# Performance work log

Hardware: AMD Instinct MI355X
Metric: run time of the kernel (lower is better)

## Reference

```python
import jax, jax.numpy as jnp
import numpy as np

B, N, K, E, H, V = 128, 256, 4, 300, 150, 32000  # batch, nodes/tree, max children, embed, hidden, vocab
DELTA = 1.0


def setup_inputs() -> dict:
    key = jax.random.key(0)
    ks = jax.random.split(key, 8)
    query = jax.random.randint(ks[0], (B, N), 0, V, dtype=jnp.int32)
    pos = jax.random.randint(ks[1], (B, N), 0, V, dtype=jnp.int32)
    neg = jax.random.randint(ks[2], (B, N), 0, V, dtype=jnp.int32)
    # Complete K-ary tree over N nodes: children of node t are {K*t+1, ..., K*t+K} < N; root = node 0.
    ch = np.full((N, K), -1, dtype=np.int32)
    for t in range(N):
        for j in range(K):
            c = K * t + 1 + j
            if c < N:
                ch[t, j] = c
    children = jnp.asarray(ch)
    emb = jax.random.normal(ks[3], (V, E), dtype=jnp.float32) * 0.02
    W_iou = jax.random.normal(ks[4], (E, 3 * H), dtype=jnp.float32) * 0.05
    U_iou = jax.random.normal(ks[5], (H, 3 * H), dtype=jnp.float32) * 0.05
    b_iou = jnp.zeros((3 * H,), jnp.float32)
    W_f = jax.random.normal(ks[6], (E, H), dtype=jnp.float32) * 0.05
    U_f = jax.random.normal(ks[7], (H, H), dtype=jnp.float32) * 0.05
    b_f = jnp.zeros((H,), jnp.float32)
    return {"query": query, "pos": pos, "neg": neg, "children": children,
            "emb": emb, "W_iou": W_iou, "U_iou": U_iou, "b_iou": b_iou,
            "W_f": W_f, "U_f": U_f, "b_f": b_f}


def _childsum_treelstm(x, children, W_iou, U_iou, b_iou, W_f, U_f, b_f):
    """x: [B, N, E] node embeddings. Returns root (c, h): each [B, H]."""
    Bn, Nn, _ = x.shape
    Hh = U_f.shape[0]
    h0 = jnp.zeros((Bn, Nn, Hh), x.dtype)
    c0 = jnp.zeros((Bn, Nn, Hh), x.dtype)

    def step(carry, t):
        h_all, c_all = carry
        ch = children[t]                        # [K] child indices, -1 = padding
        mask = (ch >= 0)
        idx = jnp.where(mask, ch, 0)
        m = mask.astype(x.dtype)[None, :, None]  # [1, K, 1]
        h_k = h_all[:, idx] * m                 # [B, K, H]
        c_k = c_all[:, idx] * m
        h_sum = h_k.sum(axis=1)                 # child-sum h_tilde [B, H]
        x_t = x[:, t]                           # [B, E]
        iou = x_t @ W_iou + h_sum @ U_iou + b_iou
        i, o, u = jnp.split(iou, 3, axis=-1)
        i = jax.nn.sigmoid(i)
        o = jax.nn.sigmoid(o)
        u = jnp.tanh(u)
        # per-child forget gates: f_jk = sigmoid(W_f x_j + U_f h_k + b_f)
        f = jax.nn.sigmoid((x_t @ W_f + b_f)[:, None, :] + h_k @ U_f)  # [B, K, H]
        c_t = i * u + (f * c_k).sum(axis=1)     # c_k already masked
        h_t = o * jnp.tanh(c_t)
        return (h_all.at[:, t].set(h_t), c_all.at[:, t].set(c_t)), None

    # children have larger indices than parents -> process N-1 .. 0 (root last)
    (h_all, c_all), _ = jax.lax.scan(step, (h0, c0), jnp.arange(Nn - 1, -1, -1))
    return c_all[:, 0], h_all[:, 0]


def _cosine(a, b):
    num = (a * b).sum(-1)
    den = jnp.sqrt((a * a).sum(-1) * (b * b).sum(-1)) + 1e-8
    return num / den


def reference(query, pos, neg, children, emb, W_iou, U_iou, b_iou, W_f, U_f, b_f):
    qc, _ = _childsum_treelstm(emb[query], children, W_iou, U_iou, b_iou, W_f, U_f, b_f)
    pc, _ = _childsum_treelstm(emb[pos], children, W_iou, U_iou, b_iou, W_f, U_f, b_f)
    nc, _ = _childsum_treelstm(emb[neg], children, W_iou, U_iou, b_iou, W_f, U_f, b_f)
    a = _cosine(qc, pc)  # [B]
    b = _cosine(qc, nc)  # [B]
    return jax.nn.relu(DELTA - a + b)
```

## Files before the change

kernel.cpp:

```cpp
#include <hip/hip_runtime.h>
#include <hip/hip_bf16.h>

typedef short short8 __attribute__((ext_vector_type(8)));
typedef float floatx4 __attribute__((ext_vector_type(4)));
typedef unsigned short ushort;

#define Bb 128
#define Nn 256
#define Hh 150
#define HK 160
#define Vv 32000
#define NROW 384
#define PROJC 600
#define NINT 64
#define ZROW (Vv + NROW * NINT)

#define WTN 640

__device__ __forceinline__ float sigf(float x) { return 1.0f / (1.0f + __expf(-x)); }
__device__ __forceinline__ float tanhf_(float x) { return 1.0f - 2.0f / (__expf(2.0f * x) + 1.0f); }
__device__ __forceinline__ float bf2f(ushort s) { union { float f; unsigned u; } v; v.u = ((unsigned)s) << 16; return v.f; }
__device__ __forceinline__ ushort f2bf(float f) { __hip_bfloat16 h = __float2bfloat16(f); return *(ushort*)&h; }

__global__ __launch_bounds__(256) void k_prep(
    const float* __restrict__ W_iou, const float* __restrict__ W_f,
    const float* __restrict__ U_iou, const float* __restrict__ U_f,
    const float* __restrict__ b_iou, const float* __restrict__ b_f,
    short* __restrict__ Wt, short* __restrict__ Uti, short* __restrict__ Utf,
    float* __restrict__ biasw, ushort* __restrict__ h_u, float* __restrict__ c_u)
{
    int idx = blockIdx.x * 256 + threadIdx.x;
    const int nWt = 320 * WTN, nUi = 160 * 464, nUf = 160 * 160;
    if (idx < nWt) {
        int k = idx / WTN, n = idx % WTN;
        float v = 0.f;
        if (k < 300) { if (n < 450) v = W_iou[k * 450 + n]; else if (n < 600) v = W_f[k * 150 + (n - 450)]; }
        Wt[n * 320 + k] = (short)f2bf(v);
    } else if (idx < nWt + nUi) {
        int i2 = idx - nWt; int k = i2 / 464, n = i2 % 464;
        float v = (k < 150 && n < 450) ? U_iou[k * 450 + n] : 0.f;
        Uti[n * 160 + k] = (short)f2bf(v);
    } else if (idx < nWt + nUi + nUf) {
        int i2 = idx - nWt - nUi; int k = i2 / 160, n = i2 % 160;
        float v = (k < 150 && n < 150) ? U_f[k * 150 + n] : 0.f;
        Utf[n * 160 + k] = (short)f2bf(v);
    } else if (idx < nWt + nUi + nUf + WTN) {
        int n = idx - nWt - nUi - nUf;
        biasw[n] = n < 450 ? b_iou[n] : (n < 600 ? b_f[n - 450] : 0.f);
    } else if (idx < nWt + nUi + nUf + WTN + HK) {
        int k = idx - (nWt + nUi + nUf + WTN);
        h_u[(long)ZROW * HK + k] = 0;
        c_u[(long)ZROW * HK + k] = 0.f;
    }
}

__global__ __launch_bounds__(256) void k_vproj(
    const float* __restrict__ emb, const short* __restrict__ Wt,
    const float* __restrict__ biasw, ushort* __restrict__ proj)
{
    __shared__ __align__(16) short As[2][32][328];
    const int tid = threadIdx.x;

    const int bid = blockIdx.x;
    const int xcd = bid & 7, li = bid >> 3;
    const int wgid = (xcd < 4 ? xcd * 63 : 252 + (xcd - 4) * 62) + li;

    const int cg = wgid % 5;
    const int rg = wgid / 5;
    const int rowbase = rg * 320;

    const int w = tid >> 6, lane = tid & 63;
    const int m = lane & 15, kq = (lane >> 4) * 8;
    const int t0 = cg * 8 + w * 2;
    const int col0 = t0 * 16 + m;
    const int col1 = col0 + 16;

    short8 bq0[10], bq1[10];
    #pragma unroll
    for (int ks = 0; ks < 10; ks++) {
        bq0[ks] = *(const short8*)(Wt + (long)col0 * 320 + kq + ks * 32);
        bq1[ks] = *(const short8*)(Wt + (long)col1 * 320 + kq + ks * 32);
    }
    const float bias0 = biasw[col0];
    const float bias1 = biasw[col1];

    for (int i = tid; i < 2 * 32 * 5; i += 256) {
        int bz = i / 160, r2 = (i % 160) / 5, kk = (i % 5) * 4;
        *(short4*)&As[bz][r2][300 + kk] = make_short4(0, 0, 0, 0);
    }

    {
        const float4* src = (const float4*)emb + (long)rowbase * 75;
        for (int i = tid; i < 2400; i += 256) {
            int r = i / 75, k0 = (i % 75) * 4;
            float4 x = src[i];
            short4 sv;
            sv.x = (short)f2bf(x.x); sv.y = (short)f2bf(x.y);
            sv.z = (short)f2bf(x.z); sv.w = (short)f2bf(x.w);
            *(short4*)&As[0][r][k0] = sv;
        }
    }
    __syncthreads();

    for (int c = 0; c < 10; c++) {
        const int buf = c & 1;

        float4 x[10];
        if (c < 9) {
            const float4* src = (const float4*)emb + (long)(rowbase + (c + 1) * 32) * 75;
            #pragma unroll
            for (int j = 0; j < 10; j++) {
                int i = tid + j * 256;
                if (i < 2400) x[j] = src[i];
            }
        }

        floatx4 a00 = {0.f,0.f,0.f,0.f}, a01 = a00, a10 = a00, a11 = a00;
        #pragma unroll
        for (int ks = 0; ks < 10; ks++) {
            short8 a0 = *(const short8*)&As[buf][m][kq + ks * 32];
            short8 a1 = *(const short8*)&As[buf][16 + m][kq + ks * 32];
            a00 = __builtin_amdgcn_mfma_f32_16x16x32_bf16(a0, bq0[ks], a00, 0, 0, 0);
            a01 = __builtin_amdgcn_mfma_f32_16x16x32_bf16(a0, bq1[ks], a01, 0, 0, 0);
            a10 = __builtin_amdgcn_mfma_f32_16x16x32_bf16(a1, bq0[ks], a10, 0, 0, 0);
            a11 = __builtin_amdgcn_mfma_f32_16x16x32_bf16(a1, bq1[ks], a11, 0, 0, 0);
        }

        {
            int v0 = rowbase + c * 32;
            int rb = (lane >> 4) * 4;
            if (col0 < PROJC) {
                #pragma unroll
                for (int reg = 0; reg < 4; reg++) {
                    proj[(long)(v0 + rb + reg) * PROJC + col0]      = f2bf(a00[reg] + bias0);
                    proj[(long)(v0 + 16 + rb + reg) * PROJC + col0] = f2bf(a10[reg] + bias0);
                }
            }
            if (col1 < PROJC) {
                #pragma unroll
                for (int reg = 0; reg < 4; reg++) {
                    proj[(long)(v0 + rb + reg) * PROJC + col1]      = f2bf(a01[reg] + bias1);
                    proj[(long)(v0 + 16 + rb + reg) * PROJC + col1] = f2bf(a11[reg] + bias1);
                }
            }
        }

        if (c < 9) {
            #pragma unroll
            for (int j = 0; j < 10; j++) {
                int i = tid + j * 256;
                if (i < 2400) {
                    int r = i / 75, k0 = (i % 75) * 4;
                    short4 sv;
                    sv.x = (short)f2bf(x[j].x); sv.y = (short)f2bf(x[j].y);
                    sv.z = (short)f2bf(x[j].z); sv.w = (short)f2bf(x[j].w);
                    *(short4*)&As[buf ^ 1][r][k0] = sv;
                }
            }
        }
        __syncthreads();
    }
}

__global__ __launch_bounds__(256) void k_vleaf(
    const ushort* __restrict__ proj, ushort* __restrict__ h_u, float* __restrict__ c_u)
{
    int idx = blockIdx.x * 256 + threadIdx.x;
    int v = idx / 20, k0 = (idx % 20) * 8;
    const ushort* pr = proj + (long)v * PROJC;
    ushort hv[8]; float cvv[8];
    #pragma unroll
    for (int e = 0; e < 8; e++) {
        int k = k0 + e;
        if (k < Hh) {
            float iv = sigf(bf2f(pr[k]));
            float ov = sigf(bf2f(pr[150 + k]));
            float uv = tanhf_(bf2f(pr[300 + k]));
            float cc = iv * uv;
            cvv[e] = cc;
            hv[e] = f2bf(ov * tanhf_(cc));
        } else { cvv[e] = 0.f; hv[e] = 0; }
    }
    *(int4*)(h_u + (long)v * HK + k0) = *(int4*)hv;
    *(float4*)(c_u + (long)v * HK + k0)     = make_float4(cvv[0], cvv[1], cvv[2], cvv[3]);
    *(float4*)(c_u + (long)v * HK + k0 + 4) = make_float4(cvv[4], cvv[5], cvv[6], cvv[7]);
}

__device__ __forceinline__ void level_step(
    int tA, int nT, int r0,
    const int* __restrict__ tq, const int* __restrict__ tp, const int* __restrict__ tn,
    const int* __restrict__ children, const ushort* __restrict__ proj,
    const short* __restrict__ Uti, const short* __restrict__ Utf,
    ushort* __restrict__ h_u, float* __restrict__ c_u,
    short (*As)[16][168] ,
    ushort (*idx_s)[16][4], ushort (*tok_s)[16])
{
    const int tid = threadIdx.x;

    if (tid < 64 * nT) {
        int tt = tid >> 6, q = tid & 63;
        int r = q >> 2, j = q & 3;
        int t = tA + tt;
        int rg = r0 + r, g = rg >> 7, b = rg & 127;
        const int* tok = (g == 0) ? tq : (g == 1 ? tp : tn);
        int ch = children[t * 4 + j];
        int idx;
        if (ch < 0)        idx = ZROW;
        else if (ch >= 64) idx = tok[b * Nn + ch];
        else               idx = Vv + rg * NINT + ch;
        idx_s[tt][r][j] = (ushort)idx;
        if (j == 0) tok_s[tt][r] = (ushort)tok[b * Nn + t];
    }
    __syncthreads();

    for (int i = tid; i < 320 * nT; i += 256) {
        int tt = i / 320, i2 = i % 320;
        int r = i2 / 20, k0 = (i2 % 20) * 8;
        int4 v0 = *(const int4*)(h_u + (long)idx_s[tt][r][0] * HK + k0);
        int4 v1 = *(const int4*)(h_u + (long)idx_s[tt][r][1] * HK + k0);
        int4 v2 = *(const int4*)(h_u + (long)idx_s[tt][r][2] * HK + k0);
        int4 v3 = *(const int4*)(h_u + (long)idx_s[tt][r][3] * HK + k0);
        *(int4*)&As[tt * 5 + 1][r][k0] = v0;
        *(int4*)&As[tt * 5 + 2][r][k0] = v1;
        *(int4*)&As[tt * 5 + 3][r][k0] = v2;
        *(int4*)&As[tt * 5 + 4][r][k0] = v3;
        ushort s[8];
        const ushort* p0 = (const ushort*)&v0; const ushort* p1 = (const ushort*)&v1;
        const ushort* p2 = (const ushort*)&v2; const ushort* p3 = (const ushort*)&v3;
        #pragma unroll
        for (int e = 0; e < 8; e++)
            s[e] = f2bf(bf2f(p0[e]) + bf2f(p1[e]) + bf2f(p2[e]) + bf2f(p3[e]));
        *(int4*)&As[tt * 5 + 0][r][k0] = *(int4*)s;
    }
    __syncthreads();

    const int w = tid >> 6, lane = tid & 63;
    const int m = lane & 15, kq = (lane >> 4) * 8;
    const int rbase = (lane >> 4) * 4;

    for (int nt = w; nt < 10; nt += 4) {
        int col = nt * 16 + m;

        short8 Bi[5], Bo[5], Bu[5], Bf[5];
        #pragma unroll
        for (int ks = 0; ks < 5; ks++) {
            Bi[ks] = *(const short8*)(Uti + (long)(col)       * HK + kq + ks * 32);
            Bo[ks] = *(const short8*)(Uti + (long)(150 + col) * HK + kq + ks * 32);
            Bu[ks] = *(const short8*)(Uti + (long)(300 + col) * HK + kq + ks * 32);
            Bf[ks] = *(const short8*)(Utf + (long)(col)       * HK + kq + ks * 32);
        }

        for (int tt = 0; tt < nT; ++tt) {
            int t = tA + tt;

            float pv0[4], pv1[4], pv2[4], pv3[4];
            float cu0[4], cu1[4], cu2[4], cu3[4];
            if (col < Hh) {
                #pragma unroll
                for (int reg = 0; reg < 4; reg++) {
                    const ushort* pr = proj + (long)tok_s[tt][rbase + reg] * PROJC;
                    pv0[reg] = bf2f(pr[col]);
                    pv1[reg] = bf2f(pr[150 + col]);
                    pv2[reg] = bf2f(pr[300 + col]);
                    pv3[reg] = bf2f(pr[450 + col]);
                    cu0[reg] = c_u[(long)idx_s[tt][rbase + reg][0] * HK + col];
                    cu1[reg] = c_u[(long)idx_s[tt][rbase + reg][1] * HK + col];
                    cu2[reg] = c_u[(long)idx_s[tt][rbase + reg][2] * HK + col];
                    cu3[reg] = c_u[(long)idx_s[tt][rbase + reg][3] * HK + col];
                }
            }

            floatx4 ai = {0.f,0.f,0.f,0.f}, ao = ai, au = ai;
            floatx4 af0 = ai, af1 = ai, af2 = ai, af3 = ai;
            #pragma unroll
            for (int ks = 0; ks < 5; ks++) {
                short8 asum = *(const short8*)&As[tt * 5 + 0][m][kq + ks * 32];
                short8 ac0  = *(const short8*)&As[tt * 5 + 1][m][kq + ks * 32];
                short8 ac1  = *(const short8*)&As[tt * 5 + 2][m][kq + ks * 32];
                short8 ac2  = *(const short8*)&As[tt * 5 + 3][m][kq + ks * 32];
                short8 ac3  = *(const short8*)&As[tt * 5 + 4][m][kq + ks * 32];
                ai  = __builtin_amdgcn_mfma_f32_16x16x32_bf16(asum, Bi[ks], ai, 0, 0, 0);
                ao  = __builtin_amdgcn_mfma_f32_16x16x32_bf16(asum, Bo[ks], ao, 0, 0, 0);
                au  = __builtin_amdgcn_mfma_f32_16x16x32_bf16(asum, Bu[ks], au, 0, 0, 0);
                af0 = __builtin_amdgcn_mfma_f32_16x16x32_bf16(ac0,  Bf[ks], af0, 0, 0, 0);
                af1 = __builtin_amdgcn_mfma_f32_16x16x32_bf16(ac1,  Bf[ks], af1, 0, 0, 0);
                af2 = __builtin_amdgcn_mfma_f32_16x16x32_bf16(ac2,  Bf[ks], af2, 0, 0, 0);
                af3 = __builtin_amdgcn_mfma_f32_16x16x32_bf16(ac3,  Bf[ks], af3, 0, 0, 0);
            }

            if (col < Hh) {
                #pragma unroll
                for (int reg = 0; reg < 4; reg++) {
                    int rg = r0 + rbase + reg;
                    float iv = sigf(pv0[reg] + ai[reg]);
                    float ov = sigf(pv1[reg] + ao[reg]);
                    float uv = tanhf_(pv2[reg] + au[reg]);
                    float fpre = pv3[reg];
                    float cv = iv * uv;
                    cv = fmaf(sigf(fpre + af0[reg]), cu0[reg], cv);
                    cv = fmaf(sigf(fpre + af1[reg]), cu1[reg], cv);
                    cv = fmaf(sigf(fpre + af2[reg]), cu2[reg], cv);
                    cv = fmaf(sigf(fpre + af3[reg]), cu3[reg], cv);
                    long o = (long)(Vv + rg * NINT + t) * HK + col;
                    c_u[o] = cv;
                    h_u[o] = f2bf(ov * tanhf_(cv));
                }
            } else {
                #pragma unroll
                for (int reg = 0; reg < 4; reg++) {
                    long o = (long)(Vv + (r0 + rbase + reg) * NINT + t) * HK + col;
                    c_u[o] = 0.f; h_u[o] = 0;
                }
            }
        }
    }
}

__global__ __launch_bounds__(256) void k_level(
    int t_base, int t_cnt,
    const int* __restrict__ tq, const int* __restrict__ tp, const int* __restrict__ tn,
    const int* __restrict__ children, const ushort* __restrict__ proj,
    const short* __restrict__ Uti, const short* __restrict__ Utf,
    ushort* __restrict__ h_u, float* __restrict__ c_u)
{
    __shared__ __align__(16) short As[10][16][168];
    __shared__ ushort idx_s[2][16][4];
    __shared__ ushort tok_s[2][16];

    const int chunk = blockIdx.x / 24;
    const int r0 = (blockIdx.x % 24) * 16;
    const int tA = t_base + chunk * 2;
    const int nT = min(2, t_base + t_cnt - tA);

    level_step(tA, nT, r0, tq, tp, tn, children, proj, Uti, Utf, h_u, c_u,
               As, idx_s, tok_s);
}

__global__ __launch_bounds__(256) void k_l34(
    const int* __restrict__ tq, const int* __restrict__ tp, const int* __restrict__ tn,
    const int* __restrict__ children, const ushort* __restrict__ proj,
    const short* __restrict__ Uti, const short* __restrict__ Utf,
    ushort* __restrict__ h_u, float* __restrict__ c_u)
{
    __shared__ __align__(16) short As[10][16][168];
    __shared__ ushort idx_s[2][16][4];
    __shared__ ushort tok_s[2][16];

    const int r0 = blockIdx.x * 16;

    level_step(1, 2, r0, tq, tp, tn, children, proj, Uti, Utf, h_u, c_u,
               As, idx_s, tok_s);
    __syncthreads();
    level_step(3, 2, r0, tq, tp, tn, children, proj, Uti, Utf, h_u, c_u,
               As, idx_s, tok_s);
    __syncthreads();
    level_step(0, 1, r0, tq, tp, tn, children, proj, Uti, Utf, h_u, c_u,
               As, idx_s, tok_s);
}

__global__ __launch_bounds__(64) void k_cos(const float* __restrict__ c_u, float* __restrict__ out)
{
    int b = blockIdx.x, tid = threadIdx.x;
    const float* qc = c_u + (long)(Vv + (0 * Bb + b) * NINT) * HK;
    const float* pc = c_u + (long)(Vv + (1 * Bb + b) * NINT) * HK;
    const float* nc = c_u + (long)(Vv + (2 * Bb + b) * NINT) * HK;
    float qp = 0, qn = 0, qq = 0, pp = 0, nn2 = 0;
    for (int k = tid; k < Hh; k += 64) {
        float qv = qc[k], pv = pc[k], nv = nc[k];
        qp += qv * pv; qn += qv * nv; qq += qv * qv; pp += pv * pv; nn2 += nv * nv;
    }
    #pragma unroll
    for (int off = 32; off > 0; off >>= 1) {
        qp += __shfl_down(qp, off, 64);
        qn += __shfl_down(qn, off, 64);
        qq += __shfl_down(qq, off, 64);
        pp += __shfl_down(pp, off, 64);
        nn2 += __shfl_down(nn2, off, 64);
    }
    if (tid == 0) {
        float a = qp / (sqrtf(qq * pp) + 1e-8f);
        float d = qn / (sqrtf(qq * nn2) + 1e-8f);
        out[b] = fmaxf(0.0f, 1.0f - a + d);
    }
}

extern "C" void kernel_launch(void* const* d_in, const int* in_sizes, int n_in,
                              void* d_out, int out_size, void* d_ws, size_t ws_size,
                              hipStream_t stream)
{
    const int*   tq       = (const int*)d_in[0];
    const int*   tp       = (const int*)d_in[1];
    const int*   tn       = (const int*)d_in[2];
    const int*   children = (const int*)d_in[3];
    const float* emb      = (const float*)d_in[4];
    const float* W_iou    = (const float*)d_in[5];
    const float* U_iou    = (const float*)d_in[6];
    const float* b_iou    = (const float*)d_in[7];
    const float* W_f      = (const float*)d_in[8];
    const float* U_f      = (const float*)d_in[9];
    const float* b_f      = (const float*)d_in[10];
    float* out = (float*)d_out;

    char* ws = (char*)d_ws;
    ushort* proj  = (ushort*)ws;
    ushort* h_u   = (ushort*)(ws + 38400000);
    float*  c_u   = (float*)(ws + 56504640);
    short*  Wt    = (short*)(ws + 92713920);
    short*  Uti   = (short*)(ws + 93123520);
    short*  Utf   = (short*)(ws + 93272000);
    float*  biasw = (float*)(ws + 93323200);

    k_prep<<<1194, 256, 0, stream>>>(W_iou, W_f, U_iou, U_f, b_iou, b_f,
                                     Wt, Uti, Utf, biasw, h_u, c_u);
    k_vproj<<<500, 256, 0, stream>>>(emb, Wt, biasw, proj);
    k_vleaf<<<2500, 256, 0, stream>>>(proj, h_u, c_u);
    k_level<<<22 * 24, 256, 0, stream>>>(21, 43, tq, tp, tn, children, proj, Uti, Utf, h_u, c_u);
    k_level<<<8 * 24, 256, 0, stream>>>(5, 16, tq, tp, tn, children, proj, Uti, Utf, h_u, c_u);
    k_l34<<<24, 256, 0, stream>>>(tq, tp, tn, children, proj, Uti, Utf, h_u, c_u);
    k_cos<<<Bb, 64, 0, stream>>>(c_u, out);
}
```

Before: 263.3 us.

## Split top tree levels across column-block workgroups instead of one fused kernel

The single 24-block kernel that ran levels 1-4 and the root sequentially is replaced by two launches of a templated level kernel. Each launch splits the hidden-column tiles across two workgroups per row group, so the small top levels run on more blocks. This trades one fused launch and its in-block barriers for an extra kernel launch plus duplicated child gathering in each column-split block.

After: 240.8 us. 1.09x faster.

```diff
diff --git a/kernel.cpp b/kernel.cpp
--- a/kernel.cpp
+++ b/kernel.cpp
@@ -186,14 +186,14 @@
     *(float4*)(c_u + (long)v * HK + k0 + 4) = make_float4(cvv[4], cvv[5], cvv[6], cvv[7]);
 }
 
+template<int CB>
 __device__ __forceinline__ void level_step(
-    int tA, int nT, int r0,
+    int tA, int nT, int r0, int cb,
     const int* __restrict__ tq, const int* __restrict__ tp, const int* __restrict__ tn,
     const int* __restrict__ children, const ushort* __restrict__ proj,
     const short* __restrict__ Uti, const short* __restrict__ Utf,
     ushort* __restrict__ h_u, float* __restrict__ c_u,
-    short (*As)[16][168] ,
-    ushort (*idx_s)[16][4], ushort (*tok_s)[16])
+    short (*As)[16][168], ushort (*idx_s)[16][4], ushort (*tok_s)[16])
 {
     const int tid = threadIdx.x;
 
@@ -238,7 +238,7 @@
     const int m = lane & 15, kq = (lane >> 4) * 8;
     const int rbase = (lane >> 4) * 4;
 
-    for (int nt = w; nt < 10; nt += 4) {
+    for (int nt = w + 4 * cb; nt < 10; nt += 4 * CB) {
         int col = nt * 16 + m;
 
         short8 Bi[5], Bo[5], Bu[5], Bf[5];
@@ -316,6 +316,7 @@
     }
 }
 
+template<int CB>
 __global__ __launch_bounds__(256) void k_level(
     int t_base, int t_cnt,
     const int* __restrict__ tq, const int* __restrict__ tp, const int* __restrict__ tn,
@@ -327,35 +328,15 @@
     __shared__ ushort idx_s[2][16][4];
     __shared__ ushort tok_s[2][16];
 
-    const int chunk = blockIdx.x / 24;
-    const int r0 = (blockIdx.x % 24) * 16;
+    const int chunk = blockIdx.x / (24 * CB);
+    const int rem   = blockIdx.x % (24 * CB);
+    const int r0 = (rem / CB) * 16;
+    const int cb = rem % CB;
     const int tA = t_base + chunk * 2;
     const int nT = min(2, t_base + t_cnt - tA);
 
-    level_step(tA, nT, r0, tq, tp, tn, children, proj, Uti, Utf, h_u, c_u,
-               As, idx_s, tok_s);
-}
-
-__global__ __launch_bounds__(256) void k_l34(
-    const int* __restrict__ tq, const int* __restrict__ tp, const int* __restrict__ tn,
-    const int* __restrict__ children, const ushort* __restrict__ proj,
-    const short* __restrict__ Uti, const short* __restrict__ Utf,
-    ushort* __restrict__ h_u, float* __restrict__ c_u)
-{
-    __shared__ __align__(16) short As[10][16][168];
-    __shared__ ushort idx_s[2][16][4];
-    __shared__ ushort tok_s[2][16];
-
-    const int r0 = blockIdx.x * 16;
-
-    level_step(1, 2, r0, tq, tp, tn, children, proj, Uti, Utf, h_u, c_u,
-               As, idx_s, tok_s);
-    __syncthreads();
-    level_step(3, 2, r0, tq, tp, tn, children, proj, Uti, Utf, h_u, c_u,
-               As, idx_s, tok_s);
-    __syncthreads();
-    level_step(0, 1, r0, tq, tp, tn, children, proj, Uti, Utf, h_u, c_u,
-               As, idx_s, tok_s);
+    level_step<CB>(tA, nT, r0, cb, tq, tp, tn, children, proj, Uti, Utf,
+                   h_u, c_u, As, idx_s, tok_s);
 }
 
 __global__ __launch_bounds__(64) void k_cos(const float* __restrict__ c_u, float* __restrict__ out)
@@ -414,8 +395,9 @@
                                      Wt, Uti, Utf, biasw, h_u, c_u);
     k_vproj<<<500, 256, 0, stream>>>(emb, Wt, biasw, proj);
     k_vleaf<<<2500, 256, 0, stream>>>(proj, h_u, c_u);
-    k_level<<<22 * 24, 256, 0, stream>>>(21, 43, tq, tp, tn, children, proj, Uti, Utf, h_u, c_u);
-    k_level<<<8 * 24, 256, 0, stream>>>(5, 16, tq, tp, tn, children, proj, Uti, Utf, h_u, c_u);
-    k_l34<<<24, 256, 0, stream>>>(tq, tp, tn, children, proj, Uti, Utf, h_u, c_u);
+    k_level<1><<<22 * 24, 256, 0, stream>>>(21, 43, tq, tp, tn, children, proj, Uti, Utf, h_u, c_u);
+    k_level<1><<<8 * 24, 256, 0, stream>>>(5, 16, tq, tp, tn, children, proj, Uti, Utf, h_u, c_u);
+    k_level<2><<<2 * 24 * 2, 256, 0, stream>>>(1, 4, tq, tp, tn, children, proj, Uti, Utf, h_u, c_u);
+    k_level<2><<<1 * 24 * 2, 256, 0, stream>>>(0, 1, tq, tp, tn, children, proj, Uti, Utf, h_u, c_u);
     k_cos<<<Bb, 64, 0, stream>>>(c_u, out);
 }
```
